# Kernel optimization log

Measured on AMD Instinct MI355X. Metric: run time of the kernel, lower is better.

The kernel has to match this reference:

```python
import itertools
import jax, jax.numpy as jnp
import numpy as np

H, W = 512, 512
B, G, F, C = 2, 4, 9, 3
N = H * W


def _morton(pos):
    # pos: [N,3] int; interleave bits as in MortonFromPosition
    pos = np.asarray(pos, dtype=np.int32)
    code = np.zeros(len(pos), dtype=np.int64)
    coeff = np.asarray([4, 2, 1], dtype=np.int64)
    for b in range(21):
        code |= ((pos & (1 << b)) << (2 * b)) @ coeff
    return code


def _build_graph(h, w):
    xindex, yindex = np.meshgrid(np.arange(w), np.arange(h))
    xy = np.stack([yindex, xindex], axis=2).reshape(-1, 2)
    z = np.zeros((len(xy), 1), dtype=np.int64)
    hc = _morton(np.concatenate([xy, z], axis=1))
    order = np.argsort(hc)
    xy = xy[order]
    hc = hc[order]
    order_inv = np.zeros(len(xy), dtype=np.int32)
    order_inv[order] = np.arange(len(xy))
    deltas = np.array(list(itertools.product([-1, 0, 1], [-1, 0, 1])), dtype=np.int32)
    T = len(deltas)
    node_i = np.repeat(np.arange(len(xy), dtype=np.int32), T)
    loc_j = (xy[:, None, :] + deltas[None, :, :]).reshape(-1, 2)
    zc = np.zeros((len(loc_j), 1), dtype=np.int64)
    hj = _morton(np.concatenate([loc_j, zc], axis=1))
    pos = np.clip(np.searchsorted(hc, hj), 0, len(hc) - 1)
    valid = (hc[pos] == hj) & (loc_j[:, 0] >= 0) & (loc_j[:, 0] < h) \
            & (loc_j[:, 1] >= 0) & (loc_j[:, 1] < w)
    edges = np.stack([node_i[valid], pos[valid].astype(np.int32)], axis=1)
    return edges, order.astype(np.int32), order_inv


def setup_inputs() -> dict:
    key = jax.random.key(0)
    k1, k2, k3 = jax.random.split(key, 3)
    edges_np, order_np, order_inv_np = _build_graph(H, W)
    M_DIAG_INIT = 0.4
    multiM = jnp.eye(F, dtype=jnp.float32)[None, :, :] * M_DIAG_INIT
    multiM = jnp.tile(multiM, (G, 1, 1))
    return {
        "img_features": jax.random.normal(k1, (B, G, F, H, W), dtype=jnp.float32),
        "signals2d": jax.random.normal(k2, (B, G, C, H, W), dtype=jnp.float32),
        "multiM": multiM + 0.01 * jax.random.normal(k3, (G, F, F), dtype=jnp.float32),
        "edges": jnp.asarray(edges_np, dtype=jnp.int32),
        "order": jnp.asarray(order_np, dtype=jnp.int32),
        "order_inverse": jnp.asarray(order_inv_np, dtype=jnp.int32),
    }


def reference(img_features, signals2d, multiM, edges, order, order_inverse):
    b, g, f, h, w = img_features.shape
    n = h * w
    # F.normalize over feature dim (eps=1e-12)
    norm = jnp.sqrt(jnp.sum(img_features * img_features, axis=2, keepdims=True))
    feats = img_features / jnp.maximum(norm, 1e-12)
    # signal2D_to_graph_signals: flatten + Morton reorder
    node_feats = feats.reshape(b, g, f, n)[..., order]          # [b,g,f,n]
    fM = jnp.einsum('bgcn,gcv->bgvn', node_feats, multiM)        # [b,g,f,n]
    nodeI = edges[:, 0]
    nodeJ = edges[:, 1]
    sim = jnp.sum(fM[..., nodeI] * fM[..., nodeJ], axis=2)       # [b,g,E]
    ew = jnp.exp(jnp.clip(sim, -10.0, 10.0))                     # [b,g,E]
    # degree = scatter-add of edge weights by source node (== one-hot buffer sum)
    deg = jnp.zeros((b, g, n), dtype=ew.dtype).at[:, :, nodeI].add(ew)
    dinv = 1.0 / jnp.sqrt(deg)
    ew_n = dinv[:, :, nodeI] * ew * dinv[:, :, nodeJ]            # [b,g,E]
    # op_L_norm on graph signals
    sig = signals2d.reshape(b, g, -1, n)[..., order]             # [b,g,c,n]
    se = sig[..., nodeJ] * ew_n[:, :, None, :]                   # [b,g,c,E]
    agg = jnp.zeros_like(sig).at[:, :, :, nodeI].add(se)
    out = sig - agg
    # graph_signals_to_signal2D
    out2d = out[..., order_inverse].reshape(b, g, -1, h, w)
    return out2d
```

## Files before the change

kernel.cpp:

```cpp
#include <hip/hip_runtime.h>
#include <hip/hip_fp16.h>

#define Hh 512
#define Ww 512
#define Bb 2
#define Gg 4
#define Ff 9
#define Cc 3
#define Nn (Hh*Ww)

#define TILE 32
#define RS 36
#define DS 34
#define NT 256

struct FmPt { __half2 a0, a1, b0, b1, c; };

__device__ __forceinline__ float dotfm(const FmPt& p, const FmPt& q) {
    __half2 acc = __hmul2(p.a0, q.a0);
    acc = __hfma2(p.a1, q.a1, acc);
    acc = __hfma2(p.b0, q.b0, acc);
    acc = __hfma2(p.b1, q.b1, acc);
    acc = __hfma2(p.c,  q.c,  acc);
    return __low2float(acc) + __high2float(acc);
}

__device__ __forceinline__ float ew_of(float s) {
    s = fminf(fmaxf(s, -10.f), 10.f);
    return __expf(s);
}

#define PXOUT(ev, I0, J0, A0, A1, A2) do {                                   \
    __half2 agg01 = __floats2half2_rn(0.f, 0.f);                             \
    __half2 agg2v = __floats2half2_rn(0.f, 0.f);                             \
    float dp = dvf[((I0) + 1) * 4 + ((J0) + 1)];                             \
    _Pragma("unroll")                                                        \
    for (int j9 = 0; j9 < 9; ++j9) {                                         \
        int k = ((I0) + j9 / 3) * 4 + ((J0) + j9 % 3);                       \
        float wf = dp * ev[j9] * dvf[k];                                     \
        __half2 wh = __float2half2_rn(wf);                                   \
        agg01 = __hfma2(wh, s01[k], agg01);                                  \
        agg2v = __hfma2(wh, s2d[k], agg2v);   \
    }                                                                        \
    A0 = __low2float(agg01); A1 = __high2float(agg01);                       \
    A2 = __low2float(agg2v);                                                 \
} while (0)

__global__ void __launch_bounds__(NT, 4) fused_kernel(const float* __restrict__ img,
                                                      const float* __restrict__ M,
                                                      const float* __restrict__ sig,
                                                      float* __restrict__ out) {
    __shared__ __half2 fmA[RS * RS][2];
    __shared__ __half2 fmB[RS * RS][2];
    __shared__ __half2 fmC[RS * RS];
    __shared__ __half  sgdv[DS * DS][4];

    const int tid = threadIdx.x;
    const int bg   = blockIdx.x & 7;
    const int tile = blockIdx.x >> 3;
    const int g    = bg & (Gg - 1);
    const int by0  = (tile >> 4) * TILE;
    const int bx0  = (tile & 15) * TILE;
    const bool border = (by0 == 0) | (by0 == Hh - TILE) | (bx0 == 0) | (bx0 == Ww - TILE);

    const float* imgP = img + (size_t)bg * Ff * Nn;
    const float* sgp  = sig + (size_t)bg * Cc * Nn;
    const float* Mg   = M + g * Ff * Ff;

    auto LD = [&](int idx) -> FmPt {
        FmPt p;
        p.a0 = fmA[idx][0]; p.a1 = fmA[idx][1];
        p.b0 = fmB[idx][0]; p.b1 = fmB[idx][1];
        p.c  = fmC[idx];
        return p;
    };

    for (int i = tid; i < DS * DS; i += NT) {
        unsigned r = (unsigned)i / DS, c = (unsigned)i - r * DS;
        int gy = by0 - 1 + (int)r, gx = bx0 - 1 + (int)c;
        float v0 = 0.f, v1 = 0.f, v2 = 0.f;
        if ((unsigned)gy < Hh && (unsigned)gx < Ww) {
            int q = gy * Ww + gx;
            v0 = sgp[q]; v1 = sgp[Nn + q]; v2 = sgp[2 * Nn + q];
        }
        *(__half2*)&sgdv[i][0] = __floats2half2_rn(v0, v1);
        *(__half2*)&sgdv[i][2] = __floats2half2_rn(v2, 0.f);
    }

    for (int i = tid; i < RS * RS; i += NT) {
        unsigned r = (unsigned)i / RS, c = (unsigned)i - r * RS;
        int gy = by0 - 2 + (int)r, gx = bx0 - 2 + (int)c;
        float m[Ff];
        if ((unsigned)gy < Hh && (unsigned)gx < Ww) {
            const float* src = imgP + gy * Ww + gx;
            float v[Ff]; float ss = 0.f;
#pragma unroll
            for (int f = 0; f < Ff; ++f) { v[f] = src[f * Nn]; ss += v[f] * v[f]; }
            float inv = 1.0f / fmaxf(sqrtf(ss), 1e-12f);
#pragma unroll
            for (int f = 0; f < Ff; ++f) v[f] *= inv;
#pragma unroll
            for (int vv = 0; vv < Ff; ++vv) {
                float acc = 0.f;
#pragma unroll
                for (int cc = 0; cc < Ff; ++cc) acc = fmaf(v[cc], Mg[cc * Ff + vv], acc);
                m[vv] = acc;
            }
        } else {
#pragma unroll
            for (int f = 0; f < Ff; ++f) m[f] = 0.f;
        }
        fmA[i][0] = __floats2half2_rn(m[0], m[1]);
        fmA[i][1] = __floats2half2_rn(m[2], m[3]);
        fmB[i][0] = __floats2half2_rn(m[4], m[5]);
        fmB[i][1] = __floats2half2_rn(m[6], m[7]);
        fmC[i]    = __floats2half2_rn(m[8], 0.f);
    }
    __syncthreads();

    const int r2 = tid >> 4, c2 = tid & 15;
    const int gy0 = by0 + 2 * r2, gx0 = bx0 + 2 * c2;
    const int wb  = (2 * r2 + 1) * RS + (2 * c2 + 1);

    FmPt w0[4], w1[4], w2[4], w3[4];
#pragma unroll
    for (int ci = 0; ci < 4; ++ci) w0[ci] = LD(wb + ci);
#pragma unroll
    for (int ci = 0; ci < 4; ++ci) w1[ci] = LD(wb + RS + ci);
#pragma unroll
    for (int ci = 0; ci < 4; ++ci) w2[ci] = LD(wb + 2 * RS + ci);

    float e0[9], e1[9], e2[9], e3[9];
    e0[0] = ew_of(dotfm(w1[1], w0[0])); e0[1] = ew_of(dotfm(w1[1], w0[1])); e0[2] = ew_of(dotfm(w1[1], w0[2]));
    e0[3] = ew_of(dotfm(w1[1], w1[0])); e0[4] = ew_of(dotfm(w1[1], w1[1])); e0[5] = ew_of(dotfm(w1[1], w1[2]));
    e0[6] = ew_of(dotfm(w1[1], w2[0])); e0[7] = ew_of(dotfm(w1[1], w2[1])); e0[8] = ew_of(dotfm(w1[1], w2[2]));
    e1[0] = ew_of(dotfm(w1[2], w0[1])); e1[1] = ew_of(dotfm(w1[2], w0[2])); e1[2] = ew_of(dotfm(w1[2], w0[3]));
    e1[3] = e0[5];                      e1[4] = ew_of(dotfm(w1[2], w1[2])); e1[5] = ew_of(dotfm(w1[2], w1[3]));
    e1[6] = ew_of(dotfm(w1[2], w2[1])); e1[7] = ew_of(dotfm(w1[2], w2[2])); e1[8] = ew_of(dotfm(w1[2], w2[3]));

#pragma unroll
    for (int ci = 0; ci < 4; ++ci) w3[ci] = LD(wb + 3 * RS + ci);

    e2[0] = ew_of(dotfm(w2[1], w1[0])); e2[1] = e0[7];                      e2[2] = e1[6];
    e2[3] = ew_of(dotfm(w2[1], w2[0])); e2[4] = ew_of(dotfm(w2[1], w2[1])); e2[5] = ew_of(dotfm(w2[1], w2[2]));
    e2[6] = ew_of(dotfm(w2[1], w3[0])); e2[7] = ew_of(dotfm(w2[1], w3[1])); e2[8] = ew_of(dotfm(w2[1], w3[2]));
    e3[0] = e0[8];                      e3[1] = e1[7];                      e3[2] = ew_of(dotfm(w2[2], w1[3]));
    e3[3] = e2[5];                      e3[4] = ew_of(dotfm(w2[2], w2[2])); e3[5] = ew_of(dotfm(w2[2], w2[3]));
    e3[6] = ew_of(dotfm(w2[2], w3[1])); e3[7] = ew_of(dotfm(w2[2], w3[2])); e3[8] = ew_of(dotfm(w2[2], w3[3]));

    if (border) {
#pragma unroll
        for (int j = 0; j < 9; ++j) {
            int dy = j / 3 - 1, dx = j % 3 - 1;
            if (!(((unsigned)(gy0 + dy)     < Hh) & ((unsigned)(gx0 + dx)     < Ww))) e0[j] = 0.f;
            if (!(((unsigned)(gy0 + dy)     < Hh) & ((unsigned)(gx0 + 1 + dx) < Ww))) e1[j] = 0.f;
            if (!(((unsigned)(gy0 + 1 + dy) < Hh) & ((unsigned)(gx0 + dx)     < Ww))) e2[j] = 0.f;
            if (!(((unsigned)(gy0 + 1 + dy) < Hh) & ((unsigned)(gx0 + 1 + dx) < Ww))) e3[j] = 0.f;
        }
    }

    float deg0 = 0.f, deg1 = 0.f, deg2 = 0.f, deg3 = 0.f;
#pragma unroll
    for (int j = 0; j < 9; ++j) { deg0 += e0[j]; deg1 += e1[j]; deg2 += e2[j]; deg3 += e3[j]; }
    {
        const int db = (2 * r2 + 1) * DS + (2 * c2 + 1);
        sgdv[db][3]          = __float2half_rn(1.0f / sqrtf(deg0));
        sgdv[db + 1][3]      = __float2half_rn(1.0f / sqrtf(deg1));
        sgdv[db + DS][3]     = __float2half_rn(1.0f / sqrtf(deg2));
        sgdv[db + DS + 1][3] = __float2half_rn(1.0f / sqrtf(deg3));
    }

    if (tid < 132) {
        int r, c;
        if (tid < 34)       { r = 0;        c = tid;       }
        else if (tid < 68)  { r = 33;       c = tid - 34;  }
        else if (tid < 100) { r = tid - 67; c = 0;         }
        else                { r = tid - 99; c = 33;        }
        int gy = by0 - 1 + r, gx = bx0 - 1 + c;
        float d = 1.0f;
        if ((unsigned)gy < Hh && (unsigned)gx < Ww) {
            int fi = (r + 1) * RS + (c + 1);
            FmPt a = LD(fi);
            float deg = 0.f;
#pragma unroll
            for (int j = 0; j < 9; ++j) {
                int dy = j / 3 - 1, dx = j % 3 - 1;
                FmPt q = LD(fi + dy * RS + dx);
                float e = ew_of(dotfm(a, q));
                bool valid = ((unsigned)(gy + dy) < Hh) & ((unsigned)(gx + dx) < Ww);
                deg += valid ? e : 0.f;
            }
            d = 1.0f / sqrtf(deg);
        }
        sgdv[r * DS + c][3] = __float2half_rn(d);
    }
    __syncthreads();

    const int sb = 2 * r2 * DS + 2 * c2;
    __half2 s01[16], s2d[16]; float dvf[16];
#pragma unroll
    for (int k = 0; k < 16; ++k) {
        int idx = sb + (k >> 2) * DS + (k & 3);
        s01[k] = *(const __half2*)&sgdv[idx][0];
        s2d[k] = *(const __half2*)&sgdv[idx][2];
        dvf[k] = __half2float(__high2half(s2d[k]));
    }

    float a00, a01, a02, a10, a11, a12, a20, a21, a22, a30, a31, a32;
    PXOUT(e0, 0, 0, a00, a01, a02);
    PXOUT(e1, 0, 1, a10, a11, a12);
    PXOUT(e2, 1, 0, a20, a21, a22);
    PXOUT(e3, 1, 1, a30, a31, a32);

    float* o = out + (size_t)bg * Cc * Nn;
    {
        int p = gy0 * Ww + gx0;
        float2 s0 = *(const float2*)&sgp[p];
        float2 s1 = *(const float2*)&sgp[Nn + p];
        float2 s2 = *(const float2*)&sgp[2 * Nn + p];
        *(float2*)&o[p]          = make_float2(s0.x - a00, s0.y - a10);
        *(float2*)&o[Nn + p]     = make_float2(s1.x - a01, s1.y - a11);
        *(float2*)&o[2 * Nn + p] = make_float2(s2.x - a02, s2.y - a12);
        p += Ww;
        s0 = *(const float2*)&sgp[p];
        s1 = *(const float2*)&sgp[Nn + p];
        s2 = *(const float2*)&sgp[2 * Nn + p];
        *(float2*)&o[p]          = make_float2(s0.x - a20, s0.y - a30);
        *(float2*)&o[Nn + p]     = make_float2(s1.x - a21, s1.y - a31);
        *(float2*)&o[2 * Nn + p] = make_float2(s2.x - a22, s2.y - a32);
    }
}

extern "C" void kernel_launch(void* const* d_in, const int* in_sizes, int n_in,
                              void* d_out, int out_size, void* d_ws, size_t ws_size,
                              hipStream_t stream) {
    const float* img = (const float*)d_in[0];
    const float* sig = (const float*)d_in[1];
    const float* M   = (const float*)d_in[2];
    float* out = (float*)d_out;

    fused_kernel<<<dim3(256 * Bb * Gg), NT, 0, stream>>>(img, M, sig, out);
}
```

Before: 40.15 us.

## Read signal neighbours from global memory, pad LDS rows, keep fp32 aggregation

The shared-memory staging of the signal halo is removed. Each thread now loads its 4x4 neighbourhood of each signal channel straight from global memory, with clamped indices, and aggregates in fp32 FMAs instead of packed half2. LDS row strides get one element of padding to avoid bank conflicts, the degree-inverse array becomes fp32, the ninth feature is stored as a single half, and launch bounds are raised to 5 blocks per SM. This cuts LDS use and a sync-phase loop in exchange for redundant, partly uncoalesced global reads that rely on the cache, and higher register pressure.

Result: faster. 38.03 us (-5.3%).

```diff
diff --git a/kernel.cpp b/kernel.cpp
--- a/kernel.cpp
+++ b/kernel.cpp
@@ -11,18 +11,19 @@
 
 #define TILE 32
 #define RS 36
+#define RSP 37
 #define DS 34
+#define DSP 35
 #define NT 256
 
-struct FmPt { __half2 a0, a1, b0, b1, c; };
+struct FmPt { __half2 a0, a1, b0, b1; float cf; };
 
 __device__ __forceinline__ float dotfm(const FmPt& p, const FmPt& q) {
     __half2 acc = __hmul2(p.a0, q.a0);
     acc = __hfma2(p.a1, q.a1, acc);
     acc = __hfma2(p.b0, q.b0, acc);
     acc = __hfma2(p.b1, q.b1, acc);
-    acc = __hfma2(p.c,  q.c,  acc);
-    return __low2float(acc) + __high2float(acc);
+    return __low2float(acc) + __high2float(acc) + p.cf * q.cf;
 }
 
 __device__ __forceinline__ float ew_of(float s) {
@@ -30,30 +31,14 @@
     return __expf(s);
 }
 
-#define PXOUT(ev, I0, J0, A0, A1, A2) do {                                   \
-    __half2 agg01 = __floats2half2_rn(0.f, 0.f);                             \
-    __half2 agg2v = __floats2half2_rn(0.f, 0.f);                             \
-    float dp = dvf[((I0) + 1) * 4 + ((J0) + 1)];                             \
-    _Pragma("unroll")                                                        \
-    for (int j9 = 0; j9 < 9; ++j9) {                                         \
-        int k = ((I0) + j9 / 3) * 4 + ((J0) + j9 % 3);                       \
-        float wf = dp * ev[j9] * dvf[k];                                     \
-        __half2 wh = __float2half2_rn(wf);                                   \
-        agg01 = __hfma2(wh, s01[k], agg01);                                  \
-        agg2v = __hfma2(wh, s2d[k], agg2v);   \
-    }                                                                        \
-    A0 = __low2float(agg01); A1 = __high2float(agg01);                       \
-    A2 = __low2float(agg2v);                                                 \
-} while (0)
-
-__global__ void __launch_bounds__(NT, 4) fused_kernel(const float* __restrict__ img,
+__global__ void __launch_bounds__(NT, 5) fused_kernel(const float* __restrict__ img,
                                                       const float* __restrict__ M,
                                                       const float* __restrict__ sig,
                                                       float* __restrict__ out) {
-    __shared__ __half2 fmA[RS * RS][2];
-    __shared__ __half2 fmB[RS * RS][2];
-    __shared__ __half2 fmC[RS * RS];
-    __shared__ __half  sgdv[DS * DS][4];
+    __shared__ __half2 fmA[RS * RSP][2];
+    __shared__ __half2 fmB[RS * RSP][2];
+    __shared__ __half  fmC[RS * RSP];
+    __shared__ float   dv[DS * DSP];
 
     const int tid = threadIdx.x;
     const int bg   = blockIdx.x & 7;
@@ -71,21 +56,9 @@
         FmPt p;
         p.a0 = fmA[idx][0]; p.a1 = fmA[idx][1];
         p.b0 = fmB[idx][0]; p.b1 = fmB[idx][1];
-        p.c  = fmC[idx];
+        p.cf = __half2float(fmC[idx]);
         return p;
     };
-
-    for (int i = tid; i < DS * DS; i += NT) {
-        unsigned r = (unsigned)i / DS, c = (unsigned)i - r * DS;
-        int gy = by0 - 1 + (int)r, gx = bx0 - 1 + (int)c;
-        float v0 = 0.f, v1 = 0.f, v2 = 0.f;
-        if ((unsigned)gy < Hh && (unsigned)gx < Ww) {
-            int q = gy * Ww + gx;
-            v0 = sgp[q]; v1 = sgp[Nn + q]; v2 = sgp[2 * Nn + q];
-        }
-        *(__half2*)&sgdv[i][0] = __floats2half2_rn(v0, v1);
-        *(__half2*)&sgdv[i][2] = __floats2half2_rn(v2, 0.f);
-    }
 
     for (int i = tid; i < RS * RS; i += NT) {
         unsigned r = (unsigned)i / RS, c = (unsigned)i - r * RS;
@@ -110,25 +83,26 @@
 #pragma unroll
             for (int f = 0; f < Ff; ++f) m[f] = 0.f;
         }
-        fmA[i][0] = __floats2half2_rn(m[0], m[1]);
-        fmA[i][1] = __floats2half2_rn(m[2], m[3]);
-        fmB[i][0] = __floats2half2_rn(m[4], m[5]);
-        fmB[i][1] = __floats2half2_rn(m[6], m[7]);
-        fmC[i]    = __floats2half2_rn(m[8], 0.f);
+        int si = r * RSP + c;
+        fmA[si][0] = __floats2half2_rn(m[0], m[1]);
+        fmA[si][1] = __floats2half2_rn(m[2], m[3]);
+        fmB[si][0] = __floats2half2_rn(m[4], m[5]);
+        fmB[si][1] = __floats2half2_rn(m[6], m[7]);
+        fmC[si]    = __float2half_rn(m[8]);
     }
     __syncthreads();
 
     const int r2 = tid >> 4, c2 = tid & 15;
     const int gy0 = by0 + 2 * r2, gx0 = bx0 + 2 * c2;
-    const int wb  = (2 * r2 + 1) * RS + (2 * c2 + 1);
+    const int wb  = (2 * r2 + 1) * RSP + (2 * c2 + 1);
 
     FmPt w0[4], w1[4], w2[4], w3[4];
 #pragma unroll
     for (int ci = 0; ci < 4; ++ci) w0[ci] = LD(wb + ci);
 #pragma unroll
-    for (int ci = 0; ci < 4; ++ci) w1[ci] = LD(wb + RS + ci);
-#pragma unroll
-    for (int ci = 0; ci < 4; ++ci) w2[ci] = LD(wb + 2 * RS + ci);
+    for (int ci = 0; ci < 4; ++ci) w1[ci] = LD(wb + RSP + ci);
+#pragma unroll
+    for (int ci = 0; ci < 4; ++ci) w2[ci] = LD(wb + 2 * RSP + ci);
 
     float e0[9], e1[9], e2[9], e3[9];
     e0[0] = ew_of(dotfm(w1[1], w0[0])); e0[1] = ew_of(dotfm(w1[1], w0[1])); e0[2] = ew_of(dotfm(w1[1], w0[2]));
@@ -139,7 +113,7 @@
     e1[6] = ew_of(dotfm(w1[2], w2[1])); e1[7] = ew_of(dotfm(w1[2], w2[2])); e1[8] = ew_of(dotfm(w1[2], w2[3]));
 
 #pragma unroll
-    for (int ci = 0; ci < 4; ++ci) w3[ci] = LD(wb + 3 * RS + ci);
+    for (int ci = 0; ci < 4; ++ci) w3[ci] = LD(wb + 3 * RSP + ci);
 
     e2[0] = ew_of(dotfm(w2[1], w1[0])); e2[1] = e0[7];                      e2[2] = e1[6];
     e2[3] = ew_of(dotfm(w2[1], w2[0])); e2[4] = ew_of(dotfm(w2[1], w2[1])); e2[5] = ew_of(dotfm(w2[1], w2[2]));
@@ -163,11 +137,11 @@
 #pragma unroll
     for (int j = 0; j < 9; ++j) { deg0 += e0[j]; deg1 += e1[j]; deg2 += e2[j]; deg3 += e3[j]; }
     {
-        const int db = (2 * r2 + 1) * DS + (2 * c2 + 1);
-        sgdv[db][3]          = __float2half_rn(1.0f / sqrtf(deg0));
-        sgdv[db + 1][3]      = __float2half_rn(1.0f / sqrtf(deg1));
-        sgdv[db + DS][3]     = __float2half_rn(1.0f / sqrtf(deg2));
-        sgdv[db + DS + 1][3] = __float2half_rn(1.0f / sqrtf(deg3));
+        const int db = (2 * r2 + 1) * DSP + (2 * c2 + 1);
+        dv[db]           = 1.0f / sqrtf(deg0);
+        dv[db + 1]       = 1.0f / sqrtf(deg1);
+        dv[db + DSP]     = 1.0f / sqrtf(deg2);
+        dv[db + DSP + 1] = 1.0f / sqrtf(deg3);
     }
 
     if (tid < 132) {
@@ -179,55 +153,67 @@
         int gy = by0 - 1 + r, gx = bx0 - 1 + c;
         float d = 1.0f;
         if ((unsigned)gy < Hh && (unsigned)gx < Ww) {
-            int fi = (r + 1) * RS + (c + 1);
+            int fi = (r + 1) * RSP + (c + 1);
             FmPt a = LD(fi);
             float deg = 0.f;
 #pragma unroll
             for (int j = 0; j < 9; ++j) {
                 int dy = j / 3 - 1, dx = j % 3 - 1;
-                FmPt q = LD(fi + dy * RS + dx);
+                FmPt q = LD(fi + dy * RSP + dx);
                 float e = ew_of(dotfm(a, q));
                 bool valid = ((unsigned)(gy + dy) < Hh) & ((unsigned)(gx + dx) < Ww);
                 deg += valid ? e : 0.f;
             }
             d = 1.0f / sqrtf(deg);
         }
-        sgdv[r * DS + c][3] = __float2half_rn(d);
+        dv[r * DSP + c] = d;
     }
     __syncthreads();
 
-    const int sb = 2 * r2 * DS + 2 * c2;
-    __half2 s01[16], s2d[16]; float dvf[16];
-#pragma unroll
-    for (int k = 0; k < 16; ++k) {
-        int idx = sb + (k >> 2) * DS + (k & 3);
-        s01[k] = *(const __half2*)&sgdv[idx][0];
-        s2d[k] = *(const __half2*)&sgdv[idx][2];
-        dvf[k] = __half2float(__high2half(s2d[k]));
-    }
-
-    float a00, a01, a02, a10, a11, a12, a20, a21, a22, a30, a31, a32;
-    PXOUT(e0, 0, 0, a00, a01, a02);
-    PXOUT(e1, 0, 1, a10, a11, a12);
-    PXOUT(e2, 1, 0, a20, a21, a22);
-    PXOUT(e3, 1, 1, a30, a31, a32);
+    float dvf[16];
+    {
+        const int db = 2 * r2 * DSP + 2 * c2;
+#pragma unroll
+        for (int k = 0; k < 16; ++k)
+            dvf[k] = dv[db + (k >> 2) * DSP + (k & 3)];
+    }
+    const float dp0 = dvf[5], dp1 = dvf[6], dp2 = dvf[9], dp3 = dvf[10];
+#pragma unroll
+    for (int j = 0; j < 9; ++j) {
+        const int k0 = (j / 3) * 4 + (j % 3);
+        e0[j] = dp0 * e0[j] * dvf[k0];
+        e1[j] = dp1 * e1[j] * dvf[k0 + 1];
+        e2[j] = dp2 * e2[j] * dvf[k0 + 4];
+        e3[j] = dp3 * e3[j] * dvf[k0 + 5];
+    }
+
+    int ry[4], cx[4];
+#pragma unroll
+    for (int i = 0; i < 4; ++i) {
+        ry[i] = min(max(gy0 - 1 + i, 0), Hh - 1) * Ww;
+        cx[i] = min(max(gx0 - 1 + i, 0), Ww - 1);
+    }
 
     float* o = out + (size_t)bg * Cc * Nn;
-    {
-        int p = gy0 * Ww + gx0;
-        float2 s0 = *(const float2*)&sgp[p];
-        float2 s1 = *(const float2*)&sgp[Nn + p];
-        float2 s2 = *(const float2*)&sgp[2 * Nn + p];
-        *(float2*)&o[p]          = make_float2(s0.x - a00, s0.y - a10);
-        *(float2*)&o[Nn + p]     = make_float2(s1.x - a01, s1.y - a11);
-        *(float2*)&o[2 * Nn + p] = make_float2(s2.x - a02, s2.y - a12);
-        p += Ww;
-        s0 = *(const float2*)&sgp[p];
-        s1 = *(const float2*)&sgp[Nn + p];
-        s2 = *(const float2*)&sgp[2 * Nn + p];
-        *(float2*)&o[p]          = make_float2(s0.x - a20, s0.y - a30);
-        *(float2*)&o[Nn + p]     = make_float2(s1.x - a21, s1.y - a31);
-        *(float2*)&o[2 * Nn + p] = make_float2(s2.x - a22, s2.y - a32);
+    const int p = gy0 * Ww + gx0;
+#pragma unroll
+    for (int ch = 0; ch < Cc; ++ch) {
+        const float* sc = sgp + (size_t)ch * Nn;
+        float s[16];
+#pragma unroll
+        for (int k = 0; k < 16; ++k) s[k] = sc[ry[k >> 2] + cx[k & 3]];
+        float a0 = 0.f, a1 = 0.f, a2 = 0.f, a3 = 0.f;
+#pragma unroll
+        for (int j = 0; j < 9; ++j) {
+            const int k0 = (j / 3) * 4 + (j % 3);
+            a0 = fmaf(e0[j], s[k0],     a0);
+            a1 = fmaf(e1[j], s[k0 + 1], a1);
+            a2 = fmaf(e2[j], s[k0 + 4], a2);
+            a3 = fmaf(e3[j], s[k0 + 5], a3);
+        }
+        float* oc = o + (size_t)ch * Nn;
+        *(float2*)&oc[p]      = make_float2(s[5] - a0, s[6]  - a1);
+        *(float2*)&oc[p + Ww] = make_float2(s[9] - a2, s[10] - a3);
     }
 }
 
```
